# Kernel tuning notes

Hardware: AMD Instinct MI355X
Metric: run time of the kernel (lower is better)

Reference implementation:

```python
import jax, jax.numpy as jnp
import numpy as np

B, T, D, H = 4, 2048, 1024, 16
HD = D // H  # head_dim = 64

def setup_inputs() -> dict:
    key = jax.random.key(0)
    ks = jax.random.split(key, 5)
    s = 0.02
    return {
        "x": jax.random.normal(ks[0], (B, T, D), jnp.float32),
        "Wq": jax.random.normal(ks[1], (D, D), jnp.float32) * s,
        "Wk": jax.random.normal(ks[2], (D, D), jnp.float32) * s,
        "Wv": jax.random.normal(ks[3], (D, D), jnp.float32) * s,
        "Wo": jax.random.normal(ks[4], (D, D), jnp.float32) * s,
        "bo": jnp.zeros((D,), jnp.float32),
    }

def reference(x, Wq, Wk, Wv, Wo, bo):
    b, t, _ = x.shape
    # projections (no qkv bias), split into heads: [b, H, t, hd]
    def split_heads(y):
        return y.reshape(b, t, H, HD).transpose(0, 2, 1, 3)
    q = split_heads(x @ Wq)
    k = split_heads(x @ Wk)
    v = split_heads(x @ Wv)
    # causal attention scores, scaled by sqrt(head_dim)
    scores = jnp.einsum('bhqd,bhkd->bhqk', q, k) / jnp.sqrt(jnp.float32(HD))
    causal = jnp.tril(jnp.ones((t, t), bool))  # True = keep
    scores = jnp.where(causal, scores, -jnp.inf)
    w = jax.nn.softmax(scores, axis=-1)
    # dropout p=0.0 -> identity (eval-mode math)
    z = jnp.einsum('bhqk,bhkd->bhqd', w, v)
    z = z.transpose(0, 2, 1, 3).reshape(b, t, D)
    return z @ Wo + bo
```

## Files before the change

kernel.cpp:

```cpp
#include <hip/hip_runtime.h>
#include <hip/hip_bf16.h>

#define B_ 4
#define T_ 2048
#define D_ 1024
#define H_ 16
#define HD_ 64
#define M_ (B_*T_)

#define QSCALE (0.125f * 1.44269504088896f)

typedef __bf16  bf16x8 __attribute__((ext_vector_type(8)));
typedef __bf16  bf16x4 __attribute__((ext_vector_type(4)));
typedef float   f32x4  __attribute__((ext_vector_type(4)));
typedef ushort  u16x8  __attribute__((ext_vector_type(8)));

__device__ __forceinline__ ushort f2bf(float f) {
  union { float f; uint u; } c; c.f = f;
  uint u = c.u;
  uint r = (u + 0x7FFFu + ((u >> 16) & 1u)) >> 16;
  return (ushort)r;
}

__device__ __forceinline__ void gload_lds16(const void* g, void* l) {
  __builtin_amdgcn_global_load_lds(
      (const __attribute__((address_space(1))) void*)g,
      (__attribute__((address_space(3))) void*)l, 16, 0, 0);
}

__global__ __launch_bounds__(256) void cast_bf16(const float* __restrict__ x,
                                                 ushort* __restrict__ o, int n) {
  int i = (blockIdx.x * 256 + threadIdx.x) * 8;
  if (i >= n) return;
  float4 a = *(const float4*)&x[i];
  float4 b = *(const float4*)&x[i + 4];
  u16x8 r;
  r[0] = f2bf(a.x); r[1] = f2bf(a.y); r[2] = f2bf(a.z); r[3] = f2bf(a.w);
  r[4] = f2bf(b.x); r[5] = f2bf(b.y); r[6] = f2bf(b.z); r[7] = f2bf(b.w);
  *(u16x8*)&o[i] = r;
}

__global__ __launch_bounds__(256) void transw(const float* __restrict__ W0,
                                              const float* __restrict__ W1,
                                              const float* __restrict__ W2,
                                              const float* __restrict__ W3,
                                              ushort* __restrict__ Wt) {
  __shared__ float tile[32][33];
  const float* W = (blockIdx.z == 0) ? W0 : (blockIdx.z == 1) ? W1
                  : (blockIdx.z == 2) ? W2 : W3;
  ushort* dst = Wt + (size_t)blockIdx.z * D_ * D_;
  int tx = threadIdx.x & 31, ty = threadIdx.x >> 5;
  int bx = blockIdx.x, by = blockIdx.y;
  #pragma unroll
  for (int i = 0; i < 4; ++i)
    tile[ty + i * 8][tx] = W[(by * 32 + ty + i * 8) * D_ + bx * 32 + tx];
  __syncthreads();
  #pragma unroll
  for (int i = 0; i < 4; ++i)
    dst[(bx * 32 + ty + i * 8) * D_ + by * 32 + tx] = f2bf(tile[tx][ty + i * 8]);
}

template<int EPI>
__global__ __launch_bounds__(256) void gemm_bt(const ushort* __restrict__ A,
                                               const ushort* __restrict__ Bt,
                                               const float* __restrict__ bias,
                                               ushort* __restrict__ Qb,
                                               ushort* __restrict__ Kb,
                                               ushort* __restrict__ Vt,
                                               float* __restrict__ Out) {
  __shared__ __align__(16) ushort As[128 * 64];
  __shared__ __align__(16) ushort Bs[128 * 64];
  const int tid = threadIdx.x;
  const int l   = tid & 63;
  const int wid = tid >> 6;
  const int lr  = l & 15, lg = l >> 4;
  const int wr  = wid >> 1, wc = wid & 1;

  const int nwgx = gridDim.x;
  int bid = blockIdx.y * nwgx + blockIdx.x;
  int cpx = (nwgx * gridDim.y) >> 3;
  int swz = (bid & 7) * cpx + (bid >> 3);
  const int m0 = (swz / nwgx) * 128;
  const int n0 = (swz % nwgx) * 128;

  const int srow = l >> 3;
  const int sce  = ((l & 7) ^ srow) * 8;
  const int xr   = (lr & 7) << 4;
  const int ce0  = ((0  + lg * 16) ^ xr) >> 1;
  const int ce1  = ((64 + lg * 16) ^ xr) >> 1;

  f32x4 acc[4][4];
  #pragma unroll
  for (int mi = 0; mi < 4; ++mi)
    #pragma unroll
    for (int ni = 0; ni < 4; ++ni)
      acc[mi][ni] = (f32x4){0.f, 0.f, 0.f, 0.f};

  #pragma unroll 1
  for (int k0 = 0; k0 < 1024; k0 += 64) {
    #pragma unroll
    for (int j = 0; j < 4; ++j) {
      int i = wid * 4 + j;
      int row = i * 8 + srow;
      gload_lds16(&A [(size_t)(m0 + row) * 1024 + k0 + sce], &As[i * 512]);
      gload_lds16(&Bt[(size_t)(n0 + row) * 1024 + k0 + sce], &Bs[i * 512]);
    }
    __syncthreads();
    #pragma unroll
    for (int kk = 0; kk < 2; ++kk) {
      const int ce = kk ? ce1 : ce0;
      bf16x8 af[4], bfv[4];
      #pragma unroll
      for (int mi = 0; mi < 4; ++mi)
        af[mi] = *(const bf16x8*)&As[(wr * 64 + mi * 16 + lr) * 64 + ce];
      #pragma unroll
      for (int ni = 0; ni < 4; ++ni)
        bfv[ni] = *(const bf16x8*)&Bs[(wc * 64 + ni * 16 + lr) * 64 + ce];
      #pragma unroll
      for (int mi = 0; mi < 4; ++mi)
        #pragma unroll
        for (int ni = 0; ni < 4; ++ni)
          acc[mi][ni] = __builtin_amdgcn_mfma_f32_16x16x32_bf16(
              af[mi], bfv[ni], acc[mi][ni], 0, 0, 0);
    }
    __syncthreads();
  }

  if (EPI == 0) {
    #pragma unroll
    for (int mi = 0; mi < 4; ++mi)
      #pragma unroll
      for (int ni = 0; ni < 4; ++ni) {
        int col = n0 + wc * 64 + ni * 16 + lr;
        int g = col >> 10, n = col & 1023;
        int h = n >> 6, hd = n & 63;
        #pragma unroll
        for (int r = 0; r < 4; ++r) {
          int rr = m0 + wr * 64 + mi * 16 + lg * 4 + r;
          int b = rr >> 11, t = rr & 2047;
          float v = acc[mi][ni][r];
          if (g == 0)      Qb[((b * H_ + h) * T_ + t) * HD_ + hd] = f2bf(v * QSCALE);
          else if (g == 1) Kb[((b * H_ + h) * T_ + t) * HD_ + hd] = f2bf(v);
          else             Vt[((b * H_ + h) * HD_ + hd) * T_ + t] = f2bf(v);
        }
      }
  } else {
    #pragma unroll
    for (int mi = 0; mi < 4; ++mi)
      #pragma unroll
      for (int ni = 0; ni < 4; ++ni) {
        int col = n0 + wc * 64 + ni * 16 + lr;
        float bv = bias[col];
        #pragma unroll
        for (int r = 0; r < 4; ++r) {
          int rr = m0 + wr * 64 + mi * 16 + lg * 4 + r;
          Out[(size_t)rr * 1024 + col] = acc[mi][ni][r] + bv;
        }
      }
  }
}

__global__ __launch_bounds__(256, 3) void attn_fwd(const ushort* __restrict__ Qb,
                                                   const ushort* __restrict__ Kb,
                                                   const ushort* __restrict__ Vt,
                                                   ushort* __restrict__ Z) {
  __shared__ __align__(16) ushort Ks[2][64 * 64];
  __shared__ __align__(16) ushort Vs[2][64 * 64];
  __shared__ __align__(16) ushort Plds[4][32 * 72];
  const int tid = threadIdx.x;
  const int l   = tid & 63;
  const int wid = tid >> 6;
  const int lr  = l & 15, lg = l >> 4;
  const int s   = blockIdx.x;
  const int idx = s >> 3;
  const int bh  = (s & 7) + 8 * (idx & 7);
  const int j   = 15 - (idx >> 3);
  const int q0  = j * 128;
  const int qw  = q0 + wid * 32;
  const int NT  = 2 * j + 2;
  const int myDiag = 2 * j + (wid >> 1);
  const ushort* Qh = Qb + (size_t)bh * T_ * HD_;
  const ushort* Kh = Kb + (size_t)bh * T_ * HD_;
  const ushort* Vh = Vt + (size_t)bh * HD_ * T_;
  ushort* Pl = &Plds[wid][0];

  const int srow = l >> 3;
  const int sce  = ((l & 7) ^ srow) * 8;
  const int xrE  = (lr & 7) * 8;
  const int ceK0 = (lg * 8) ^ xrE;
  const int ceK1 = (32 + lg * 8) ^ xrE;

  const int foff = lr * 64 + lg * 8;
  bf16x8 bq[2][2];
  #pragma unroll
  for (int qi = 0; qi < 2; ++qi)
    #pragma unroll
    for (int kk = 0; kk < 2; ++kk)
      bq[qi][kk] = *(const bf16x8*)&Qh[(qw + qi * 16) * 64 + kk * 32 + foff];

  f32x4 o[2][4];
  float l_[2] = {0.f, 0.f};
  #pragma unroll
  for (int mi = 0; mi < 2; ++mi)
    #pragma unroll
    for (int hi = 0; hi < 4; ++hi)
      o[mi][hi] = (f32x4){0.f, 0.f, 0.f, 0.f};

#define STAGEKV(BUF, KT)                                                        \
  {                                                                             \
    _Pragma("unroll")                                                           \
    for (int c = 0; c < 2; ++c) {                                               \
      int i = wid * 2 + c;                                                      \
      gload_lds16(&Kh[(size_t)((KT) * 64 + i * 8 + srow) * 64 + sce],           \
                  &Ks[BUF][i * 512]);                                           \
      gload_lds16(&Vh[(size_t)(i * 8 + srow) * T_ + (KT) * 64 + sce],           \
                  &Vs[BUF][i * 512]);                                           \
    }                                                                           \
  }

  STAGEKV(0, 0);
  __syncthreads();

  #pragma unroll 1
  for (int kt = 0; kt < NT; ++kt) {
    const int cur = kt & 1;
    if (kt + 1 < NT) STAGEKV(cur ^ 1, kt + 1);

    if (kt <= myDiag) {
      bf16x8 bk[4][2];
      #pragma unroll
      for (int ki = 0; ki < 4; ++ki) {
        bk[ki][0] = *(const bf16x8*)&Ks[cur][(ki * 16 + lr) * 64 + ceK0];
        bk[ki][1] = *(const bf16x8*)&Ks[cur][(ki * 16 + lr) * 64 + ceK1];
      }
      f32x4 st[4][2];
      #pragma unroll
      for (int ki = 0; ki < 4; ++ki)
        #pragma unroll
        for (int qi = 0; qi < 2; ++qi)
          st[ki][qi] = (f32x4){0.f, 0.f, 0.f, 0.f};
      __builtin_amdgcn_s_setprio(1);
      #pragma unroll
      for (int kk = 0; kk < 2; ++kk)
        #pragma unroll
        for (int ki = 0; ki < 4; ++ki)
          #pragma unroll
          for (int qi = 0; qi < 2; ++qi)
            st[ki][qi] = __builtin_amdgcn_mfma_f32_16x16x32_bf16(
                bk[ki][kk], bq[qi][kk], st[ki][qi], 0, 0, 0);
      __builtin_amdgcn_s_setprio(0);

      if (kt == myDiag) {
        const int qbase = qw - kt * 64;
        #pragma unroll
        for (int qi = 0; qi < 2; ++qi) {
          int qoff = qbase + qi * 16 + lr;
          #pragma unroll
          for (int ki = 0; ki < 4; ++ki)
            #pragma unroll
            for (int r = 0; r < 4; ++r)
              if (ki * 16 + lg * 4 + r > qoff) st[ki][qi][r] = -1e30f;
        }
      }

      #pragma unroll
      for (int qi = 0; qi < 2; ++qi) {
        float rs = 0.f;
        #pragma unroll
        for (int ki = 0; ki < 4; ++ki) {
          bf16x4 p4;
          #pragma unroll
          for (int r = 0; r < 4; ++r) {
            float p = exp2f(st[ki][qi][r]);
            rs += p;
            p4[r] = (__bf16)p;
          }
          *(bf16x4*)&Pl[(qi * 16 + lr) * 72 + ki * 16 + lg * 4] = p4;
        }
        l_[qi] += rs;
      }

      bf16x8 bv[4][2];
      #pragma unroll
      for (int hi = 0; hi < 4; ++hi) {
        bv[hi][0] = *(const bf16x8*)&Vs[cur][(hi * 16 + lr) * 64 + ceK0];
        bv[hi][1] = *(const bf16x8*)&Vs[cur][(hi * 16 + lr) * 64 + ceK1];
      }
      bf16x8 ap[2][2];
      #pragma unroll
      for (int mi = 0; mi < 2; ++mi)
        #pragma unroll
        for (int kk = 0; kk < 2; ++kk)
          ap[mi][kk] = *(const bf16x8*)&Pl[(mi * 16 + lr) * 72 + kk * 32 + lg * 8];
      __builtin_amdgcn_s_setprio(1);
      #pragma unroll
      for (int kk = 0; kk < 2; ++kk)
        #pragma unroll
        for (int mi = 0; mi < 2; ++mi)
          #pragma unroll
          for (int hi = 0; hi < 4; ++hi)
            o[mi][hi] = __builtin_amdgcn_mfma_f32_16x16x32_bf16(
                ap[mi][kk], bv[hi][kk], o[mi][hi], 0, 0, 0);
      __builtin_amdgcn_s_setprio(0);
    }
    __syncthreads();
  }
#undef STAGEKV

  #pragma unroll
  for (int mi = 0; mi < 2; ++mi) {
    l_[mi] += __shfl_xor(l_[mi], 16);
    l_[mi] += __shfl_xor(l_[mi], 32);
  }
  const int b = bh >> 4, h = bh & 15;
  #pragma unroll
  for (int mi = 0; mi < 2; ++mi)
    #pragma unroll
    for (int r = 0; r < 4; ++r) {
      float lv = __shfl(l_[mi], lg * 4 + r);
      float rinv = 1.f / lv;
      int t = qw + mi * 16 + lg * 4 + r;
      #pragma unroll
      for (int hi = 0; hi < 4; ++hi)
        Z[((size_t)(b * T_ + t)) * D_ + h * 64 + hi * 16 + lr] =
            f2bf(o[mi][hi][r] * rinv);
    }
}

extern "C" void kernel_launch(void* const* d_in, const int* in_sizes, int n_in,
                              void* d_out, int out_size, void* d_ws, size_t ws_size,
                              hipStream_t stream) {
  const float* x  = (const float*)d_in[0];
  const float* Wq = (const float*)d_in[1];
  const float* Wk = (const float*)d_in[2];
  const float* Wv = (const float*)d_in[3];
  const float* Wo = (const float*)d_in[4];
  const float* bo = (const float*)d_in[5];
  float* out = (float*)d_out;

  char* ws = (char*)d_ws;
  ushort* xb = (ushort*)(ws);
  ushort* Wt = (ushort*)(ws + 16777216);
  ushort* Qb = (ushort*)(ws + 25165824);
  ushort* Kb = (ushort*)(ws + 41943040);
  ushort* Vt = (ushort*)(ws + 58720256);
  ushort* Zb = (ushort*)(ws + 75497472);

  cast_bf16<<<4096, 256, 0, stream>>>(x, xb, M_ * D_);
  transw<<<dim3(32, 32, 4), 256, 0, stream>>>(Wq, Wk, Wv, Wo, Wt);
  gemm_bt<0><<<dim3(24, 64), 256, 0, stream>>>(xb, Wt, nullptr, Qb, Kb, Vt, nullptr);
  attn_fwd<<<1024, 256, 0, stream>>>(Qb, Kb, Vt, Zb);
  gemm_bt<1><<<dim3(8, 64), 256, 0, stream>>>(Zb, Wt + 3 * 1024 * 1024, bo,
                                              nullptr, nullptr, nullptr, out);
}
```

Measured before the change: 197.8 us.

## Triple-buffer GEMM with 256x128 tiles, 8 waves, and interleaved prefetch

Measured after the change: 185.6 us. 6.2% less time.

```diff
diff --git a/kernel.cpp b/kernel.cpp
--- a/kernel.cpp
+++ b/kernel.cpp
@@ -61,26 +61,25 @@
 }
 
 template<int EPI>
-__global__ __launch_bounds__(256) void gemm_bt(const ushort* __restrict__ A,
-                                               const ushort* __restrict__ Bt,
-                                               const float* __restrict__ bias,
-                                               ushort* __restrict__ Qb,
-                                               ushort* __restrict__ Kb,
-                                               ushort* __restrict__ Vt,
-                                               float* __restrict__ Out) {
-  __shared__ __align__(16) ushort As[128 * 64];
-  __shared__ __align__(16) ushort Bs[128 * 64];
+__global__ __launch_bounds__(512, 2) void gemm_bt(const ushort* __restrict__ A,
+                                                  const ushort* __restrict__ Bt,
+                                                  const float* __restrict__ bias,
+                                                  ushort* __restrict__ Qb,
+                                                  ushort* __restrict__ Kb,
+                                                  ushort* __restrict__ Vt,
+                                                  float* __restrict__ Out) {
+  __shared__ __align__(16) ushort S[3][24576];
   const int tid = threadIdx.x;
   const int l   = tid & 63;
   const int wid = tid >> 6;
   const int lr  = l & 15, lg = l >> 4;
-  const int wr  = wid >> 1, wc = wid & 1;
+  const int wm  = wid >> 1, wn = wid & 1;
 
   const int nwgx = gridDim.x;
   int bid = blockIdx.y * nwgx + blockIdx.x;
   int cpx = (nwgx * gridDim.y) >> 3;
   int swz = (bid & 7) * cpx + (bid >> 3);
-  const int m0 = (swz / nwgx) * 128;
+  const int m0 = (swz / nwgx) * 256;
   const int n0 = (swz % nwgx) * 128;
 
   const int srow = l >> 3;
@@ -96,64 +95,110 @@
     for (int ni = 0; ni < 4; ++ni)
       acc[mi][ni] = (f32x4){0.f, 0.f, 0.f, 0.f};
 
+#define STAGE_A(BUF, K0)                                                       \
+  { _Pragma("unroll")                                                          \
+    for (int j = 0; j < 4; ++j) {                                              \
+      int c = wid * 4 + j;                                                     \
+      gload_lds16(&A[(size_t)(m0 + c * 8 + srow) * 1024 + (K0) + sce],         \
+                  &S[BUF][c * 512]); } }
+#define STAGE_B(BUF, K0)                                                       \
+  { _Pragma("unroll")                                                          \
+    for (int j = 0; j < 2; ++j) {                                              \
+      int c = wid * 2 + j;                                                     \
+      gload_lds16(&Bt[(size_t)(n0 + c * 8 + srow) * 1024 + (K0) + sce],        \
+                  &S[BUF][16384 + c * 512]); } }
+
+  STAGE_A(0, 0);  STAGE_B(0, 0);
+  STAGE_A(1, 64); STAGE_B(1, 64);
+  asm volatile("s_waitcnt vmcnt(6)" ::: "memory");
+  __builtin_amdgcn_s_barrier();
+  __builtin_amdgcn_sched_barrier(0);
+
   #pragma unroll 1
-  for (int k0 = 0; k0 < 1024; k0 += 64) {
-    #pragma unroll
-    for (int j = 0; j < 4; ++j) {
-      int i = wid * 4 + j;
-      int row = i * 8 + srow;
-      gload_lds16(&A [(size_t)(m0 + row) * 1024 + k0 + sce], &As[i * 512]);
-      gload_lds16(&Bt[(size_t)(n0 + row) * 1024 + k0 + sce], &Bs[i * 512]);
-    }
-    __syncthreads();
-    #pragma unroll
-    for (int kk = 0; kk < 2; ++kk) {
-      const int ce = kk ? ce1 : ce0;
+  for (int t = 0; t < 16; ++t) {
+    const int cur = t % 3;
+    const int st2 = (t + 2) % 3;
+    const int k2  = (t + 2) * 64;
+    const ushort* Sa = &S[cur][0];
+    const ushort* Sb = &S[cur][16384];
+
+    {
       bf16x8 af[4], bfv[4];
       #pragma unroll
       for (int mi = 0; mi < 4; ++mi)
-        af[mi] = *(const bf16x8*)&As[(wr * 64 + mi * 16 + lr) * 64 + ce];
+        af[mi] = *(const bf16x8*)&Sa[(wm * 64 + mi * 16 + lr) * 64 + ce0];
       #pragma unroll
       for (int ni = 0; ni < 4; ++ni)
-        bfv[ni] = *(const bf16x8*)&Bs[(wc * 64 + ni * 16 + lr) * 64 + ce];
+        bfv[ni] = *(const bf16x8*)&Sb[(wn * 64 + ni * 16 + lr) * 64 + ce0];
+      if (t < 14) STAGE_A(st2, k2);
+      __builtin_amdgcn_s_barrier();
+      __builtin_amdgcn_s_setprio(1);
       #pragma unroll
       for (int mi = 0; mi < 4; ++mi)
         #pragma unroll
         for (int ni = 0; ni < 4; ++ni)
           acc[mi][ni] = __builtin_amdgcn_mfma_f32_16x16x32_bf16(
               af[mi], bfv[ni], acc[mi][ni], 0, 0, 0);
+      __builtin_amdgcn_s_setprio(0);
+      __builtin_amdgcn_s_barrier();
     }
-    __syncthreads();
+    {
+      bf16x8 af[4], bfv[4];
+      #pragma unroll
+      for (int mi = 0; mi < 4; ++mi)
+        af[mi] = *(const bf16x8*)&Sa[(wm * 64 + mi * 16 + lr) * 64 + ce1];
+      #pragma unroll
+      for (int ni = 0; ni < 4; ++ni)
+        bfv[ni] = *(const bf16x8*)&Sb[(wn * 64 + ni * 16 + lr) * 64 + ce1];
+      if (t < 14) STAGE_B(st2, k2);
+      __builtin_amdgcn_s_barrier();
+      __builtin_amdgcn_s_setprio(1);
+      #pragma unroll
+      for (int mi = 0; mi < 4; ++mi)
+        #pragma unroll
+        for (int ni = 0; ni < 4; ++ni)
+          acc[mi][ni] = __builtin_amdgcn_mfma_f32_16x16x32_bf16(
+              af[mi], bfv[ni], acc[mi][ni], 0, 0, 0);
+      __builtin_amdgcn_s_setprio(0);
+      if (t < 14)      { asm volatile("s_waitcnt vmcnt(6)" ::: "memory"); }
+      else if (t < 15) { asm volatile("s_waitcnt vmcnt(0)" ::: "memory"); }
+      if (t < 15) {
+        __builtin_amdgcn_s_barrier();
+        __builtin_amdgcn_sched_barrier(0);
+      }
+    }
   }
+#undef STAGE_A
+#undef STAGE_B
 
   if (EPI == 0) {
+    const int g = n0 >> 10;
+    const int h = ((n0 & 1023) >> 6) + wn;
     #pragma unroll
     for (int mi = 0; mi < 4; ++mi)
       #pragma unroll
+      for (int r = 0; r < 4; ++r) {
+        int rr = m0 + wm * 64 + mi * 16 + lg * 4 + r;
+        int b = rr >> 11, t = rr & 2047;
+        #pragma unroll
+        for (int ni = 0; ni < 4; ++ni) {
+          int hd = ni * 16 + lr;
+          float v = acc[mi][ni][r];
+          if (g == 0)      Qb[((size_t)(b * H_ + h) * T_ + t) * HD_ + hd] = f2bf(v * QSCALE);
+          else if (g == 1) Kb[((size_t)(b * H_ + h) * T_ + t) * HD_ + hd] = f2bf(v);
+          else             Vt[((size_t)(b * H_ + h) * HD_ + hd) * T_ + t] = f2bf(v);
+        }
+      }
+  } else {
+    #pragma unroll
+    for (int mi = 0; mi < 4; ++mi)
+      #pragma unroll
       for (int ni = 0; ni < 4; ++ni) {
-        int col = n0 + wc * 64 + ni * 16 + lr;
-        int g = col >> 10, n = col & 1023;
-        int h = n >> 6, hd = n & 63;
+        int col = n0 + wn * 64 + ni * 16 + lr;
+        float bv = bias[col];
         #pragma unroll
         for (int r = 0; r < 4; ++r) {
-          int rr = m0 + wr * 64 + mi * 16 + lg * 4 + r;
-          int b = rr >> 11, t = rr & 2047;
-          float v = acc[mi][ni][r];
-          if (g == 0)      Qb[((b * H_ + h) * T_ + t) * HD_ + hd] = f2bf(v * QSCALE);
-          else if (g == 1) Kb[((b * H_ + h) * T_ + t) * HD_ + hd] = f2bf(v);
-          else             Vt[((b * H_ + h) * HD_ + hd) * T_ + t] = f2bf(v);
-        }
-      }
-  } else {
-    #pragma unroll
-    for (int mi = 0; mi < 4; ++mi)
-      #pragma unroll
-      for (int ni = 0; ni < 4; ++ni) {
-        int col = n0 + wc * 64 + ni * 16 + lr;
-        float bv = bias[col];
-        #pragma unroll
-        for (int r = 0; r < 4; ++r) {
-          int rr = m0 + wr * 64 + mi * 16 + lg * 4 + r;
+          int rr = m0 + wm * 64 + mi * 16 + lg * 4 + r;
           Out[(size_t)rr * 1024 + col] = acc[mi][ni][r] + bv;
         }
       }
@@ -348,8 +393,8 @@
 
   cast_bf16<<<4096, 256, 0, stream>>>(x, xb, M_ * D_);
   transw<<<dim3(32, 32, 4), 256, 0, stream>>>(Wq, Wk, Wv, Wo, Wt);
-  gemm_bt<0><<<dim3(24, 64), 256, 0, stream>>>(xb, Wt, nullptr, Qb, Kb, Vt, nullptr);
+  gemm_bt<0><<<dim3(24, 32), 512, 0, stream>>>(xb, Wt, nullptr, Qb, Kb, Vt, nullptr);
   attn_fwd<<<1024, 256, 0, stream>>>(Qb, Kb, Vt, Zb);
-  gemm_bt<1><<<dim3(8, 64), 256, 0, stream>>>(Zb, Wt + 3 * 1024 * 1024, bo,
+  gemm_bt<1><<<dim3(8, 32), 512, 0, stream>>>(Zb, Wt + 3 * 1024 * 1024, bo,
                                               nullptr, nullptr, nullptr, out);
 }
```
